# Kernel tuning notes

Measured on AMD Instinct MI355X. Metric: run time of the kernel, lower is better.

## Reference

```python
import jax, jax.numpy as jnp
import numpy as np


def setup_inputs() -> dict:
    key = jax.random.key(0)
    k_x, k_w1, k_b1, k_w2, k_b2 = jax.random.split(key, 5)
    N, D, H = 4_000_000, 10, 16
    x = jax.random.normal(k_x, (N, D), dtype=jnp.float32)
    # torch.nn.Linear default init: U(-1/sqrt(fan_in), 1/sqrt(fan_in))
    lim1 = 1.0 / np.sqrt(D)
    W1 = jax.random.uniform(k_w1, (H, D), minval=-lim1, maxval=lim1, dtype=jnp.float32)
    b1 = jax.random.uniform(k_b1, (H,), minval=-lim1, maxval=lim1, dtype=jnp.float32)
    lim2 = 1.0 / np.sqrt(H)
    W2 = jax.random.uniform(k_w2, (1, H), minval=-lim2, maxval=lim2, dtype=jnp.float32)
    b2 = jax.random.uniform(k_b2, (1,), minval=-lim2, maxval=lim2, dtype=jnp.float32)
    return {"x": x, "W1": W1, "b1": b1, "W2": W2, "b2": b2}


def reference(x, W1, b1, W2, b2):
    # Gram matrix: (10, 10)
    y = x.T @ x
    # symmetric eigendecomposition; w: eigenvectors (10, 10), ascending eigenvalues
    v, w = jnp.linalg.eigh(y)
    h = jax.nn.relu(w @ W1.T + b1)          # (10, 16)
    o = h @ W2.T + b2                        # (10, 1)
    return 0.5 * (jax.nn.sigmoid(o) + 1.0)
```

## Files before the change

### kernel.cpp

```cpp
#include <hip/hip_runtime.h>
#include <math.h>

#pragma clang fp contract(off)

#define NACC 55
#define KC_DEFAULT 384
#define FOLD_LDS 12288

__device__ __forceinline__ void group_load(const float4* __restrict__ xv,
                                           long g, float4* buf) {
#pragma unroll
  for (int t = 0; t < 20; ++t) buf[t] = xv[g * 20 + t];
}

__device__ __forceinline__ void pair_fma_one(const float4 q0, const float4 q1,
                                             const float4 q2, const float4 q3,
                                             const float4 q4, float* acc) {
  float a[10] = {q0.x, q0.y, q0.z, q0.w, q1.x, q1.y, q1.z, q1.w, q2.x, q2.y};
  float b[10] = {q2.z, q2.w, q3.x, q3.y, q3.z, q3.w, q4.x, q4.y, q4.z, q4.w};
  int e = 0;
#pragma unroll
  for (int i = 0; i < 10; ++i)
#pragma unroll
    for (int j = 0; j <= i; ++j) {
      acc[e] = __builtin_fmaf(a[i], a[j], acc[e]);
      acc[e] = __builtin_fmaf(b[i], b[j], acc[e]);
      ++e;
    }
}

__device__ __forceinline__ void group_fma(const float4* buf, float* acc) {
#pragma unroll
  for (int pp = 0; pp < 4; ++pp)
    pair_fma_one(buf[pp * 5 + 0], buf[pp * 5 + 1], buf[pp * 5 + 2],
                 buf[pp * 5 + 3], buf[pp * 5 + 4], acc);
}

__global__ __launch_bounds__(64, 1) void gram32_kernel(
    const float* __restrict__ x, float* __restrict__ partial,
    int nrows, int kc, int nchunks, int prow) {
  int c = blockIdx.x * 64 + threadIdx.x;
  if (c >= nchunks) return;
  long k0 = (long)c * kc;
  long rem = (long)nrows - k0;
  int klen = rem < kc ? (int)rem : kc;

  float acc[NACC];
#pragma unroll
  for (int e = 0; e < NACC; ++e) acc[e] = 0.0f;

  const float4* __restrict__ xv = (const float4*)(x + k0 * 10);
  int npair = klen >> 1;
  int ngrp = npair >> 2;

  float4 bufA[20], bufB[20];

  int g = 0;
  if (ngrp > 0) group_load(xv, 0, bufA);
  while (g < ngrp) {
    if (g + 1 < ngrp) group_load(xv, g + 1, bufB);
    group_fma(bufA, acc);
    ++g;
    if (g >= ngrp) break;
    if (g + 1 < ngrp) group_load(xv, g + 1, bufA);
    group_fma(bufB, acc);
    ++g;
  }
  for (int p = ngrp * 4; p < npair; ++p) {
    float4 v0 = xv[(long)p * 5 + 0];
    float4 v1 = xv[(long)p * 5 + 1];
    float4 v2 = xv[(long)p * 5 + 2];
    float4 v3 = xv[(long)p * 5 + 3];
    float4 v4 = xv[(long)p * 5 + 4];
    pair_fma_one(v0, v1, v2, v3, v4, acc);
  }
  if (klen & 1) {
    const float* row = x + (k0 + klen - 1) * 10;
    float a[10];
#pragma unroll
    for (int i = 0; i < 10; ++i) a[i] = row[i];
    int e = 0;
#pragma unroll
    for (int i = 0; i < 10; ++i)
#pragma unroll
      for (int j = 0; j <= i; ++j) {
        acc[e] = __builtin_fmaf(a[i], a[j], acc[e]);
        ++e;
      }
  }
#pragma unroll
  for (int e = 0; e < NACC; ++e)
    partial[(long)e * prow + c] = acc[e];
}

__global__ __launch_bounds__(256) void fold32_kernel(
    const float* __restrict__ partial, float* __restrict__ G, int nchunks,
    int prow) {
  __shared__ float buf[FOLD_LDS];
  int e = blockIdx.x;
  const float* p = partial + (long)e * prow;

  if (nchunks <= FOLD_LDS) {
    int n4 = nchunks >> 2;
    const float4* p4 = (const float4*)p;
    float4* b4 = (float4*)buf;
    for (int i = threadIdx.x; i < n4; i += 256) b4[i] = p4[i];
    for (int i = (n4 << 2) + threadIdx.x; i < nchunks; i += 256)
      buf[i] = p[i];
    __syncthreads();
    if (threadIdx.x == 0) {
      float s = buf[0];
      int c = 1;
      for (; c + 16 <= nchunks; c += 16) {
        float v[16];
#pragma unroll
        for (int t = 0; t < 16; ++t) v[t] = buf[c + t];
#pragma unroll
        for (int t = 0; t < 16; ++t) s = s + v[t];
      }
      for (; c < nchunks; ++c) s = s + buf[c];
      G[e] = s;
    }
  } else {
    if (threadIdx.x == 0) {
      float s = p[0];
      for (int c = 1; c < nchunks; ++c) s = s + p[c];
      G[e] = s;
    }
  }
}

__device__ __forceinline__ float s_sign(float a, float b) {
  return copysignf(fabsf(a), b);
}
__device__ __forceinline__ float slapy2(float x, float y) {
  float xa = fabsf(x), ya = fabsf(y);
  float w = fmaxf(xa, ya), z = fminf(xa, ya);
  if (z == 0.0f) return w;
  float t = z / w;
  return w * sqrtf(1.0f + t * t);
}
__device__ __forceinline__ void slartg(float f, float g, float* c, float* s,
                                       float* r) {
  if (g == 0.0f) {
    *c = 1.0f; *s = 0.0f; *r = f;
  } else if (f == 0.0f) {
    *c = 0.0f; *s = s_sign(1.0f, g); *r = fabsf(g);
  } else {
    float d = sqrtf(f * f + g * g);
    *c = fabsf(f) / d;
    *r = s_sign(d, f);
    *s = g / (*r);
  }
}
__device__ void slaev2(float a, float b, float c, float* rt1, float* rt2,
                       float* cs1, float* sn1) {
  float sm = a + c, df = a - c;
  float adf = fabsf(df);
  float tb = b + b;
  float ab = fabsf(tb);
  float acmx, acmn;
  if (fabsf(a) > fabsf(c)) { acmx = a; acmn = c; } else { acmx = c; acmn = a; }
  float rt;
  if (adf > ab) { float t = ab / adf; rt = adf * sqrtf(1.0f + t * t); }
  else if (adf < ab) { float t = adf / ab; rt = ab * sqrtf(1.0f + t * t); }
  else rt = ab * sqrtf(2.0f);
  int sgn1;
  if (sm < 0.0f) {
    *rt1 = 0.5f * (sm - rt); sgn1 = -1;
    *rt2 = (acmx / *rt1) * acmn - (b / *rt1) * b;
  } else if (sm > 0.0f) {
    *rt1 = 0.5f * (sm + rt); sgn1 = 1;
    *rt2 = (acmx / *rt1) * acmn - (b / *rt1) * b;
  } else {
    *rt1 = 0.5f * rt; *rt2 = -0.5f * rt; sgn1 = 1;
  }
  int sgn2;
  float cs;
  if (df >= 0.0f) { cs = df + rt; sgn2 = 1; } else { cs = df - rt; sgn2 = -1; }
  float acs = fabsf(cs);
  if (acs > ab) {
    float ct = -tb / cs;
    *sn1 = 1.0f / sqrtf(1.0f + ct * ct);
    *cs1 = ct * (*sn1);
  } else {
    if (ab == 0.0f) { *cs1 = 1.0f; *sn1 = 0.0f; }
    else {
      float tn = -cs / tb;
      *cs1 = 1.0f / sqrtf(1.0f + tn * tn);
      *sn1 = tn * (*cs1);
    }
  }
  if (sgn1 == sgn2) { float tn = *cs1; *cs1 = -(*sn1); *sn1 = tn; }
}

__device__ __forceinline__ float xget(const float* a, int idx) {
  float r = a[0];
#pragma unroll
  for (int k = 1; k < 10; ++k)
    if (idx == k) r = a[k];
  return r;
}
__device__ __forceinline__ void xput(float* a, int idx, float v) {
#pragma unroll
  for (int k = 0; k < 10; ++k)
    if (idx == k) a[k] = v;
}

__global__ __launch_bounds__(64) void solve_kernel(
    const float* __restrict__ Gp, const float* __restrict__ W1,
    const float* __restrict__ b1, const float* __restrict__ W2,
    const float* __restrict__ b2, float* __restrict__ out) {
  const int lane = threadIdx.x;
  const int myrow = lane < 10 ? lane : 9;

  float row[10];
#pragma unroll
  for (int c = 0; c < 10; ++c) {
    int rr = myrow >= c ? myrow : c;
    int cc = myrow >= c ? c : myrow;
    row[c] = Gp[rr * (rr + 1) / 2 + cc];
  }

  float d[10], e[10], tau[9];

#pragma unroll
  for (int i = 0; i < 9; ++i) {
    float v[10];
    {
      float myci = row[i];
#pragma unroll
      for (int k = 0; k < 10; ++k) v[k] = __shfl(myci, k, 64);
    }
    float alpha = v[i + 1];
    float xn2 = 0.0f;
#pragma unroll
    for (int k = i + 2; k < 10; ++k) xn2 = xn2 + v[k] * v[k];
    float xnorm = sqrtf(xn2);
    float taui;
    if (xnorm == 0.0f) {
      taui = 0.0f;
      e[i] = alpha;
    } else {
      float beta = -s_sign(slapy2(alpha, xnorm), alpha);
      taui = (beta - alpha) / beta;
      float sc = 1.0f / (alpha - beta);
#pragma unroll
      for (int k = i + 2; k < 10; ++k) v[k] = v[k] * sc;
      if (lane >= i + 2 && lane < 10) row[i] = row[i] * sc;
      if (lane == i) {
#pragma unroll
        for (int c = i + 2; c < 10; ++c) row[c] = row[c] * sc;
      }
      if (lane == i + 1) row[i] = beta;
      if (lane == i) row[i + 1] = beta;
      e[i] = beta;
    }
    if (taui != 0.0f) {
      v[i + 1] = 1.0f;
      float vme = (lane == i + 1)
                      ? 1.0f
                      : ((lane >= i + 2 && lane < 10) ? row[i] : 0.0f);
      float s = 0.0f;
#pragma unroll
      for (int c2 = i + 1; c2 < 10; ++c2) s = s + row[c2] * v[c2];
      float pvr = taui * s;
      float pva[10];
#pragma unroll
      for (int k = 0; k < 10; ++k) pva[k] = __shfl(pvr, k, 64);
      float dot = 0.0f;
#pragma unroll
      for (int k = i + 1; k < 10; ++k) dot = dot + pva[k] * v[k];
      float alpha2 = -0.5f * taui * dot;
      pvr = pvr + alpha2 * vme;
#pragma unroll
      for (int k = 0; k < 10; ++k) pva[k] = pva[k] + alpha2 * v[k];
      if (lane >= i + 1 && lane < 10) {
#pragma unroll
        for (int c2 = i + 1; c2 < 10; ++c2)
          row[c2] = row[c2] - (vme * pva[c2] + pvr * v[c2]);
      }
    }
    tau[i] = taui;
    d[i] = __shfl(row[i], i, 64);
  }
  d[9] = __shfl(row[9], 9, 64);

  float z[10];
#pragma unroll
  for (int rr2 = 0; rr2 < 10; ++rr2) z[rr2] = (lane == rr2) ? 1.0f : 0.0f;

  const float eps = 5.9604644775390625e-08f;
  const float eps2 = 3.5527136788005009e-15f;
  const float safmin = 1.1754943508222875e-38f;
  const int nmaxit = 300;
  int jtot = 0;
  int l1 = 0;

  while (l1 < 10) {
    if (l1 > 0) xput(e, l1 - 1, 0.0f);
    int m = 9;
    {
      bool fnd = false;
#pragma unroll
      for (int mm = 0; mm < 9; ++mm) {
        if (!fnd && mm >= l1) {
          float tst = fabsf(e[mm]);
          if (tst == 0.0f) {
            m = mm; fnd = true;
          } else if (tst <=
                     (sqrtf(fabsf(d[mm])) * sqrtf(fabsf(d[mm + 1]))) * eps) {
            e[mm] = 0.0f; m = mm; fnd = true;
          }
        }
      }
    }
    int l = l1, lsv = l, lend = m, lendsv = lend;
    l1 = m + 1;
    if (lend == l) continue;
    float anorm = 0.0f;
#pragma unroll
    for (int k = 0; k < 10; ++k)
      if (k >= l && k <= lend) anorm = fmaxf(anorm, fabsf(d[k]));
#pragma unroll
    for (int k = 0; k < 9; ++k)
      if (k >= l && k < lend) anorm = fmaxf(anorm, fabsf(e[k]));
    if (anorm == 0.0f) continue;
    if (fabsf(xget(d, lend)) < fabsf(xget(d, l))) { lend = lsv; l = lendsv; }

    if (lend > l) {
      for (;;) {
        int m2 = lend;
        if (l != lend) {
          bool fnd = false;
#pragma unroll
          for (int mm = 0; mm < 9; ++mm) {
            if (!fnd && mm >= l && mm <= lend - 1) {
              float tst = e[mm] * e[mm];
              if (tst <= (eps2 * fabsf(d[mm])) * fabsf(d[mm + 1]) + safmin) {
                m2 = mm; fnd = true;
              }
            }
          }
        }
        if (m2 < lend) xput(e, m2, 0.0f);
        float p = xget(d, l);
        if (m2 == l) {
          ++l;
          if (l <= lend) continue;
          break;
        }
        if (m2 == l + 1) {
          float rt1, rt2, cc2, ss2;
          slaev2(xget(d, l), xget(e, l), xget(d, l + 1), &rt1, &rt2, &cc2,
                 &ss2);
#pragma unroll
          for (int rr2 = 0; rr2 < 10; ++rr2) {
            float zl = __shfl(z[rr2], l, 64);
            float zl1 = __shfl(z[rr2], l + 1, 64);
            float t = zl1;
            float nj1 = cc2 * t - ss2 * zl;
            float nj = ss2 * t + cc2 * zl;
            if (lane == l) z[rr2] = nj;
            if (lane == l + 1) z[rr2] = nj1;
          }
          xput(d, l, rt1);
          xput(d, l + 1, rt2);
          xput(e, l, 0.0f);
          l += 2;
          if (l <= lend) continue;
          break;
        }
        if (jtot == nmaxit) break;
        ++jtot;
        float g = (xget(d, l + 1) - p) / (2.0f * xget(e, l));
        float r2 = slapy2(g, 1.0f);
        g = xget(d, m2) - p + (xget(e, l) / (g + s_sign(r2, g)));
        float ss = 1.0f, cc = 1.0f;
        p = 0.0f;
        float wcA[10], wsA[10];
#pragma unroll
        for (int i2 = 8; i2 >= 0; --i2) {
          if (i2 >= l && i2 <= m2 - 1) {
            float f = ss * e[i2];
            float bb = cc * e[i2];
            slartg(g, f, &cc, &ss, &r2);
            if (i2 != m2 - 1) e[i2 + 1] = r2;
            g = d[i2 + 1] - p;
            r2 = (d[i2] - g) * ss + 2.0f * cc * bb;
            p = ss * r2;
            d[i2 + 1] = g + p;
            g = cc * r2 - bb;
            wcA[i2] = cc;
            wsA[i2] = -ss;
          }
        }
#pragma unroll
        for (int j = 8; j >= 0; --j) {
          if (j >= l && j <= m2 - 1) {
            float cj = wcA[j], sj = wsA[j];
#pragma unroll
            for (int rr2 = 0; rr2 < 10; ++rr2) {
              float zj = __shfl(z[rr2], j, 64);
              float zj1 = __shfl(z[rr2], j + 1, 64);
              float t = zj1;
              float nj1 = cj * t - sj * zj;
              float nj = sj * t + cj * zj;
              if (lane == j) z[rr2] = nj;
              if (lane == j + 1) z[rr2] = nj1;
            }
          }
        }
        xput(d, l, xget(d, l) - p);
        xput(e, l, g);
      }
    } else {
      for (;;) {
        int m2 = lend;
        if (l != lend) {
          bool fnd = false;
#pragma unroll
          for (int mm = 9; mm >= 1; --mm) {
            if (!fnd && mm <= l && mm >= lend + 1) {
              float tst = e[mm - 1] * e[mm - 1];
              if (tst <= (eps2 * fabsf(d[mm])) * fabsf(d[mm - 1]) + safmin) {
                m2 = mm; fnd = true;
              }
            }
          }
        }
        if (m2 > lend) xput(e, m2 - 1, 0.0f);
        float p = xget(d, l);
        if (m2 == l) {
          --l;
          if (l >= lend) continue;
          break;
        }
        if (m2 == l - 1) {
          float rt1, rt2, cc2, ss2;
          slaev2(xget(d, l - 1), xget(e, l - 1), xget(d, l), &rt1, &rt2, &cc2,
                 &ss2);
#pragma unroll
          for (int rr2 = 0; rr2 < 10; ++rr2) {
            float zl = __shfl(z[rr2], l, 64);
            float zlm = __shfl(z[rr2], l - 1, 64);
            float t = zl;
            float nl = cc2 * t - ss2 * zlm;
            float nlm = ss2 * t + cc2 * zlm;
            if (lane == l) z[rr2] = nl;
            if (lane == l - 1) z[rr2] = nlm;
          }
          xput(d, l - 1, rt1);
          xput(d, l, rt2);
          xput(e, l - 1, 0.0f);
          l -= 2;
          if (l >= lend) continue;
          break;
        }
        if (jtot == nmaxit) break;
        ++jtot;
        float g = (xget(d, l - 1) - p) / (2.0f * xget(e, l - 1));
        float r2 = slapy2(g, 1.0f);
        g = xget(d, m2) - p + (xget(e, l - 1) / (g + s_sign(r2, g)));
        float ss = 1.0f, cc = 1.0f;
        p = 0.0f;
        float wcA[10], wsA[10];
#pragma unroll
        for (int i2 = 0; i2 <= 8; ++i2) {
          if (i2 >= m2 && i2 <= l - 1) {
            float f = ss * e[i2];
            float bb = cc * e[i2];
            slartg(g, f, &cc, &ss, &r2);
            if (i2 != m2) e[(i2 > 0) ? i2 - 1 : 0] = r2;
            g = d[i2] - p;
            r2 = (d[i2 + 1] - g) * ss + 2.0f * cc * bb;
            p = ss * r2;
            d[i2] = g + p;
            g = cc * r2 - bb;
            wcA[i2] = cc;
            wsA[i2] = ss;
          }
        }
#pragma unroll
        for (int j = 0; j <= 8; ++j) {
          if (j >= m2 && j <= l - 1) {
            float cj = wcA[j], sj = wsA[j];
#pragma unroll
            for (int rr2 = 0; rr2 < 10; ++rr2) {
              float zj = __shfl(z[rr2], j, 64);
              float zj1 = __shfl(z[rr2], j + 1, 64);
              float t = zj1;
              float nj1 = cj * t - sj * zj;
              float nj = sj * t + cj * zj;
              if (lane == j) z[rr2] = nj;
              if (lane == j + 1) z[rr2] = nj1;
            }
          }
        }
        xput(d, l, xget(d, l) - p);
        xput(e, l - 1, g);
      }
    }
  }

#pragma unroll
  for (int ii = 1; ii < 10; ++ii) {
    const int i2 = ii - 1;
    int k2 = i2;
    float pmin = d[i2];
#pragma unroll
    for (int j = ii; j < 10; ++j)
      if (d[j] < pmin) { k2 = j; pmin = d[j]; }
    if (k2 != i2) {
      xput(d, k2, d[i2]);
      d[i2] = pmin;
#pragma unroll
      for (int rr2 = 0; rr2 < 10; ++rr2) {
        float zi = __shfl(z[rr2], i2, 64);
        float zk = __shfl(z[rr2], k2, 64);
        if (lane == i2) z[rr2] = zk;
        if (lane == k2) z[rr2] = zi;
      }
    }
  }

#pragma unroll
  for (int i = 8; i >= 0; --i) {
    float taui = tau[i];
    if (taui != 0.0f) {
      float hv[10];
      {
        float myci = row[i];
#pragma unroll
        for (int k = 0; k < 10; ++k) hv[k] = __shfl(myci, k, 64);
      }
      float w = z[i + 1];
#pragma unroll
      for (int k2 = i + 2; k2 < 10; ++k2) w = w + hv[k2] * z[k2];
      w = w * taui;
      z[i + 1] = z[i + 1] - w;
#pragma unroll
      for (int k2 = i + 2; k2 < 10; ++k2) z[k2] = z[k2] - hv[k2] * w;
    }
  }

  float zrow[10];
#pragma unroll
  for (int rr2 = 0; rr2 < 10; ++rr2) {
#pragma unroll
    for (int c = 0; c < 10; ++c) {
      float t = __shfl(z[rr2], c, 64);
      if (lane == rr2) zrow[c] = t;
    }
  }

  if (lane < 10) {
    float o = 0.0f;
#pragma unroll
    for (int j = 0; j < 16; ++j) {
      float acc = 0.0f;
#pragma unroll
      for (int k = 0; k < 10; ++k) acc = acc + zrow[k] * W1[j * 10 + k];
      acc = acc + b1[j];
      float h = fmaxf(acc, 0.0f);
      o = o + h * W2[j];
    }
    o = o + b2[0];
    float sig = 1.0f / (1.0f + expf(-o));
    out[lane] = 0.5f * (sig + 1.0f);
  }
}

extern "C" void kernel_launch(void* const* d_in, const int* in_sizes, int n_in,
                              void* d_out, int out_size, void* d_ws,
                              size_t ws_size, hipStream_t stream) {
  const float* x = (const float*)d_in[0];
  const float* W1 = (const float*)d_in[1];
  const float* b1 = (const float*)d_in[2];
  const float* W2 = (const float*)d_in[3];
  const float* b2 = (const float*)d_in[4];
  float* out = (float*)d_out;

  int nrows = in_sizes[0] / 10;

  int kc = KC_DEFAULT;
  for (;;) {
    long nchunks = ((long)nrows + kc - 1) / kc;
    long prow = (nchunks + 63) & ~63L;
    size_t need = (size_t)NACC * prow * sizeof(float) + 256;
    if (need <= ws_size || kc > nrows) break;
    kc *= 2;
  }
  int nchunks = (int)(((long)nrows + kc - 1) / kc);
  int prow = (int)(((long)nchunks + 63) & ~63L);

  float* partial = (float*)d_ws;
  float* G = partial + (size_t)NACC * prow;

  int grid = (nchunks + 63) / 64;
  gram32_kernel<<<grid, 64, 0, stream>>>(x, partial, nrows, kc, nchunks,
                                         prow);
  fold32_kernel<<<NACC, 256, 0, stream>>>(partial, G, nchunks, prow);
  solve_kernel<<<1, 64, 0, stream>>>(G, W1, b1, W2, b2, out);
}
```

Baseline: 201.0 us.

## Keep eigenvector rows per lane and scalarize tridiagonal state to avoid shuffles

Switches the eigenvector accumulator from a column-per-lane layout to a row-per-lane layout held in named scalar registers, so each Givens rotation becomes local arithmetic instead of twenty cross-lane shuffles. The diagonal, off-diagonal and rotation arrays become scalar registers accessed through select-chain macros to avoid scratch memory for dynamic indexing. A single shuffle-based transpose is added before the Householder back-transformation. The select chains add ALU work per dynamic access and raise register use.

```diff
diff --git a/kernel.cpp b/kernel.cpp
--- a/kernel.cpp
+++ b/kernel.cpp
@@ -194,18 +194,16 @@
   if (sgn1 == sgn2) { float tn = *cs1; *cs1 = -(*sn1); *sn1 = tn; }
 }
 
-__device__ __forceinline__ float xget(const float* a, int idx) {
-  float r = a[0];
-#pragma unroll
-  for (int k = 1; k < 10; ++k)
-    if (idx == k) r = a[k];
-  return r;
-}
-__device__ __forceinline__ void xput(float* a, int idx, float v) {
-#pragma unroll
-  for (int k = 0; k < 10; ++k)
-    if (idx == k) a[k] = v;
-}
+#define GETD(i) ((i)==0?d0:(i)==1?d1:(i)==2?d2:(i)==3?d3:(i)==4?d4:(i)==5?d5:(i)==6?d6:(i)==7?d7:(i)==8?d8:d9)
+#define PUTD(i,v) do{int _i=(i);float _x=(v);d0=(_i==0)?_x:d0;d1=(_i==1)?_x:d1;d2=(_i==2)?_x:d2;d3=(_i==3)?_x:d3;d4=(_i==4)?_x:d4;d5=(_i==5)?_x:d5;d6=(_i==6)?_x:d6;d7=(_i==7)?_x:d7;d8=(_i==8)?_x:d8;d9=(_i==9)?_x:d9;}while(0)
+#define GETE(i) ((i)==0?e0:(i)==1?e1:(i)==2?e2:(i)==3?e3:(i)==4?e4:(i)==5?e5:(i)==6?e6:(i)==7?e7:e8)
+#define PUTE(i,v) do{int _i=(i);float _x=(v);e0=(_i==0)?_x:e0;e1=(_i==1)?_x:e1;e2=(_i==2)?_x:e2;e3=(_i==3)?_x:e3;e4=(_i==4)?_x:e4;e5=(_i==5)?_x:e5;e6=(_i==6)?_x:e6;e7=(_i==7)?_x:e7;e8=(_i==8)?_x:e8;}while(0)
+#define GETWC(i) ((i)==0?wc0:(i)==1?wc1:(i)==2?wc2:(i)==3?wc3:(i)==4?wc4:(i)==5?wc5:(i)==6?wc6:(i)==7?wc7:wc8)
+#define PUTWC(i,v) do{int _i=(i);float _x=(v);wc0=(_i==0)?_x:wc0;wc1=(_i==1)?_x:wc1;wc2=(_i==2)?_x:wc2;wc3=(_i==3)?_x:wc3;wc4=(_i==4)?_x:wc4;wc5=(_i==5)?_x:wc5;wc6=(_i==6)?_x:wc6;wc7=(_i==7)?_x:wc7;wc8=(_i==8)?_x:wc8;}while(0)
+#define GETWS(i) ((i)==0?ws0:(i)==1?ws1:(i)==2?ws2:(i)==3?ws3:(i)==4?ws4:(i)==5?ws5:(i)==6?ws6:(i)==7?ws7:ws8)
+#define PUTWS(i,v) do{int _i=(i);float _x=(v);ws0=(_i==0)?_x:ws0;ws1=(_i==1)?_x:ws1;ws2=(_i==2)?_x:ws2;ws3=(_i==3)?_x:ws3;ws4=(_i==4)?_x:ws4;ws5=(_i==5)?_x:ws5;ws6=(_i==6)?_x:ws6;ws7=(_i==7)?_x:ws7;ws8=(_i==8)?_x:ws8;}while(0)
+#define GETZ(i) ((i)==0?z0:(i)==1?z1:(i)==2?z2:(i)==3?z3:(i)==4?z4:(i)==5?z5:(i)==6?z6:(i)==7?z7:(i)==8?z8:z9)
+#define PUTZ(i,v) do{int _i=(i);float _x=(v);z0=(_i==0)?_x:z0;z1=(_i==1)?_x:z1;z2=(_i==2)?_x:z2;z3=(_i==3)?_x:z3;z4=(_i==4)?_x:z4;z5=(_i==5)?_x:z5;z6=(_i==6)?_x:z6;z7=(_i==7)?_x:z7;z8=(_i==8)?_x:z8;z9=(_i==9)?_x:z9;}while(0)
 
 __global__ __launch_bounds__(64) void solve_kernel(
     const float* __restrict__ Gp, const float* __restrict__ W1,
@@ -222,7 +220,9 @@
     row[c] = Gp[rr * (rr + 1) / 2 + cc];
   }
 
-  float d[10], e[10], tau[9];
+  float d0, d1, d2, d3, d4, d5, d6, d7, d8, d9;
+  float e0, e1, e2, e3, e4, e5, e6, e7, e8;
+  float tau[9];
 
 #pragma unroll
   for (int i = 0; i < 9; ++i) {
@@ -240,7 +240,7 @@
     float taui;
     if (xnorm == 0.0f) {
       taui = 0.0f;
-      e[i] = alpha;
+      PUTE(i, alpha);
     } else {
       float beta = -s_sign(slapy2(alpha, xnorm), alpha);
       taui = (beta - alpha) / beta;
@@ -254,7 +254,7 @@
       }
       if (lane == i + 1) row[i] = beta;
       if (lane == i) row[i + 1] = beta;
-      e[i] = beta;
+      PUTE(i, beta);
     }
     if (taui != 0.0f) {
       v[i + 1] = 1.0f;
@@ -282,13 +282,26 @@
       }
     }
     tau[i] = taui;
-    d[i] = __shfl(row[i], i, 64);
-  }
-  d[9] = __shfl(row[9], 9, 64);
-
-  float z[10];
-#pragma unroll
-  for (int rr2 = 0; rr2 < 10; ++rr2) z[rr2] = (lane == rr2) ? 1.0f : 0.0f;
+    PUTD(i, __shfl(row[i], i, 64));
+  }
+  PUTD(9, __shfl(row[9], 9, 64));
+
+  float z0, z1, z2, z3, z4, z5, z6, z7, z8, z9;
+  z0 = (lane == 0) ? 1.0f : 0.0f;
+  z1 = (lane == 1) ? 1.0f : 0.0f;
+  z2 = (lane == 2) ? 1.0f : 0.0f;
+  z3 = (lane == 3) ? 1.0f : 0.0f;
+  z4 = (lane == 4) ? 1.0f : 0.0f;
+  z5 = (lane == 5) ? 1.0f : 0.0f;
+  z6 = (lane == 6) ? 1.0f : 0.0f;
+  z7 = (lane == 7) ? 1.0f : 0.0f;
+  z8 = (lane == 8) ? 1.0f : 0.0f;
+  z9 = (lane == 9) ? 1.0f : 0.0f;
+
+  float wc0, wc1, wc2, wc3, wc4, wc5, wc6, wc7, wc8;
+  float ws0, ws1, ws2, ws3, ws4, ws5, ws6, ws7, ws8;
+  wc0 = wc1 = wc2 = wc3 = wc4 = wc5 = wc6 = wc7 = wc8 = 0.0f;
+  ws0 = ws1 = ws2 = ws3 = ws4 = ws5 = ws6 = ws7 = ws8 = 0.0f;
 
   const float eps = 5.9604644775390625e-08f;
   const float eps2 = 3.5527136788005009e-15f;
@@ -298,19 +311,20 @@
   int l1 = 0;
 
   while (l1 < 10) {
-    if (l1 > 0) xput(e, l1 - 1, 0.0f);
+    if (l1 > 0) PUTE(l1 - 1, 0.0f);
     int m = 9;
     {
       bool fnd = false;
 #pragma unroll
       for (int mm = 0; mm < 9; ++mm) {
         if (!fnd && mm >= l1) {
-          float tst = fabsf(e[mm]);
+          float tst = fabsf(GETE(mm));
           if (tst == 0.0f) {
             m = mm; fnd = true;
           } else if (tst <=
-                     (sqrtf(fabsf(d[mm])) * sqrtf(fabsf(d[mm + 1]))) * eps) {
-            e[mm] = 0.0f; m = mm; fnd = true;
+                     (sqrtf(fabsf(GETD(mm))) * sqrtf(fabsf(GETD(mm + 1)))) *
+                         eps) {
+            PUTE(mm, 0.0f); m = mm; fnd = true;
           }
         }
       }
@@ -321,12 +335,12 @@
     float anorm = 0.0f;
 #pragma unroll
     for (int k = 0; k < 10; ++k)
-      if (k >= l && k <= lend) anorm = fmaxf(anorm, fabsf(d[k]));
+      if (k >= l && k <= lend) anorm = fmaxf(anorm, fabsf(GETD(k)));
 #pragma unroll
     for (int k = 0; k < 9; ++k)
-      if (k >= l && k < lend) anorm = fmaxf(anorm, fabsf(e[k]));
+      if (k >= l && k < lend) anorm = fmaxf(anorm, fabsf(GETE(k)));
     if (anorm == 0.0f) continue;
-    if (fabsf(xget(d, lend)) < fabsf(xget(d, l))) { lend = lsv; l = lendsv; }
+    if (fabsf(GETD(lend)) < fabsf(GETD(l))) { lend = lsv; l = lendsv; }
 
     if (lend > l) {
       for (;;) {
@@ -336,15 +350,16 @@
 #pragma unroll
           for (int mm = 0; mm < 9; ++mm) {
             if (!fnd && mm >= l && mm <= lend - 1) {
-              float tst = e[mm] * e[mm];
-              if (tst <= (eps2 * fabsf(d[mm])) * fabsf(d[mm + 1]) + safmin) {
+              float tst = GETE(mm) * GETE(mm);
+              if (tst <=
+                  (eps2 * fabsf(GETD(mm))) * fabsf(GETD(mm + 1)) + safmin) {
                 m2 = mm; fnd = true;
               }
             }
           }
         }
-        if (m2 < lend) xput(e, m2, 0.0f);
-        float p = xget(d, l);
+        if (m2 < lend) PUTE(m2, 0.0f);
+        float p = GETD(l);
         if (m2 == l) {
           ++l;
           if (l <= lend) continue;
@@ -352,67 +367,57 @@
         }
         if (m2 == l + 1) {
           float rt1, rt2, cc2, ss2;
-          slaev2(xget(d, l), xget(e, l), xget(d, l + 1), &rt1, &rt2, &cc2,
-                 &ss2);
-#pragma unroll
-          for (int rr2 = 0; rr2 < 10; ++rr2) {
-            float zl = __shfl(z[rr2], l, 64);
-            float zl1 = __shfl(z[rr2], l + 1, 64);
+          slaev2(GETD(l), GETE(l), GETD(l + 1), &rt1, &rt2, &cc2, &ss2);
+          {
+            float zl = GETZ(l), zl1 = GETZ(l + 1);
             float t = zl1;
-            float nj1 = cc2 * t - ss2 * zl;
-            float nj = ss2 * t + cc2 * zl;
-            if (lane == l) z[rr2] = nj;
-            if (lane == l + 1) z[rr2] = nj1;
-          }
-          xput(d, l, rt1);
-          xput(d, l + 1, rt2);
-          xput(e, l, 0.0f);
+            float nl1 = cc2 * t - ss2 * zl;
+            float nl = ss2 * t + cc2 * zl;
+            PUTZ(l + 1, nl1);
+            PUTZ(l, nl);
+          }
+          PUTD(l, rt1);
+          PUTD(l + 1, rt2);
+          PUTE(l, 0.0f);
           l += 2;
           if (l <= lend) continue;
           break;
         }
         if (jtot == nmaxit) break;
         ++jtot;
-        float g = (xget(d, l + 1) - p) / (2.0f * xget(e, l));
+        float g = (GETD(l + 1) - p) / (2.0f * GETE(l));
         float r2 = slapy2(g, 1.0f);
-        g = xget(d, m2) - p + (xget(e, l) / (g + s_sign(r2, g)));
+        g = GETD(m2) - p + (GETE(l) / (g + s_sign(r2, g)));
         float ss = 1.0f, cc = 1.0f;
         p = 0.0f;
-        float wcA[10], wsA[10];
 #pragma unroll
         for (int i2 = 8; i2 >= 0; --i2) {
           if (i2 >= l && i2 <= m2 - 1) {
-            float f = ss * e[i2];
-            float bb = cc * e[i2];
+            float f = ss * GETE(i2);
+            float bb = cc * GETE(i2);
             slartg(g, f, &cc, &ss, &r2);
-            if (i2 != m2 - 1) e[i2 + 1] = r2;
-            g = d[i2 + 1] - p;
-            r2 = (d[i2] - g) * ss + 2.0f * cc * bb;
+            if (i2 != m2 - 1) PUTE(i2 + 1, r2);
+            g = GETD(i2 + 1) - p;
+            r2 = (GETD(i2) - g) * ss + 2.0f * cc * bb;
             p = ss * r2;
-            d[i2 + 1] = g + p;
+            PUTD(i2 + 1, g + p);
             g = cc * r2 - bb;
-            wcA[i2] = cc;
-            wsA[i2] = -ss;
+            PUTWC(i2, cc);
+            PUTWS(i2, -ss);
           }
         }
 #pragma unroll
         for (int j = 8; j >= 0; --j) {
           if (j >= l && j <= m2 - 1) {
-            float cj = wcA[j], sj = wsA[j];
-#pragma unroll
-            for (int rr2 = 0; rr2 < 10; ++rr2) {
-              float zj = __shfl(z[rr2], j, 64);
-              float zj1 = __shfl(z[rr2], j + 1, 64);
-              float t = zj1;
-              float nj1 = cj * t - sj * zj;
-              float nj = sj * t + cj * zj;
-              if (lane == j) z[rr2] = nj;
-              if (lane == j + 1) z[rr2] = nj1;
-            }
-          }
-        }
-        xput(d, l, xget(d, l) - p);
-        xput(e, l, g);
+            float cj = GETWC(j), sj = GETWS(j);
+            float t = GETZ(j + 1);
+            float zj = GETZ(j);
+            PUTZ(j + 1, cj * t - sj * zj);
+            PUTZ(j, sj * t + cj * zj);
+          }
+        }
+        PUTD(l, GETD(l) - p);
+        PUTE(l, g);
       }
     } else {
       for (;;) {
@@ -422,15 +427,16 @@
 #pragma unroll
           for (int mm = 9; mm >= 1; --mm) {
             if (!fnd && mm <= l && mm >= lend + 1) {
-              float tst = e[mm - 1] * e[mm - 1];
-              if (tst <= (eps2 * fabsf(d[mm])) * fabsf(d[mm - 1]) + safmin) {
+              float tst = GETE(mm - 1) * GETE(mm - 1);
+              if (tst <=
+                  (eps2 * fabsf(GETD(mm))) * fabsf(GETD(mm - 1)) + safmin) {
                 m2 = mm; fnd = true;
               }
             }
           }
         }
-        if (m2 > lend) xput(e, m2 - 1, 0.0f);
-        float p = xget(d, l);
+        if (m2 > lend) PUTE(m2 - 1, 0.0f);
+        float p = GETD(l);
         if (m2 == l) {
           --l;
           if (l >= lend) continue;
@@ -438,67 +444,57 @@
         }
         if (m2 == l - 1) {
           float rt1, rt2, cc2, ss2;
-          slaev2(xget(d, l - 1), xget(e, l - 1), xget(d, l), &rt1, &rt2, &cc2,
-                 &ss2);
-#pragma unroll
-          for (int rr2 = 0; rr2 < 10; ++rr2) {
-            float zl = __shfl(z[rr2], l, 64);
-            float zlm = __shfl(z[rr2], l - 1, 64);
+          slaev2(GETD(l - 1), GETE(l - 1), GETD(l), &rt1, &rt2, &cc2, &ss2);
+          {
+            float zl = GETZ(l), zlm = GETZ(l - 1);
             float t = zl;
             float nl = cc2 * t - ss2 * zlm;
             float nlm = ss2 * t + cc2 * zlm;
-            if (lane == l) z[rr2] = nl;
-            if (lane == l - 1) z[rr2] = nlm;
-          }
-          xput(d, l - 1, rt1);
-          xput(d, l, rt2);
-          xput(e, l - 1, 0.0f);
+            PUTZ(l, nl);
+            PUTZ(l - 1, nlm);
+          }
+          PUTD(l - 1, rt1);
+          PUTD(l, rt2);
+          PUTE(l - 1, 0.0f);
           l -= 2;
           if (l >= lend) continue;
           break;
         }
         if (jtot == nmaxit) break;
         ++jtot;
-        float g = (xget(d, l - 1) - p) / (2.0f * xget(e, l - 1));
+        float g = (GETD(l - 1) - p) / (2.0f * GETE(l - 1));
         float r2 = slapy2(g, 1.0f);
-        g = xget(d, m2) - p + (xget(e, l - 1) / (g + s_sign(r2, g)));
+        g = GETD(m2) - p + (GETE(l - 1) / (g + s_sign(r2, g)));
         float ss = 1.0f, cc = 1.0f;
         p = 0.0f;
-        float wcA[10], wsA[10];
 #pragma unroll
         for (int i2 = 0; i2 <= 8; ++i2) {
           if (i2 >= m2 && i2 <= l - 1) {
-            float f = ss * e[i2];
-            float bb = cc * e[i2];
+            float f = ss * GETE(i2);
+            float bb = cc * GETE(i2);
             slartg(g, f, &cc, &ss, &r2);
-            if (i2 != m2) e[(i2 > 0) ? i2 - 1 : 0] = r2;
-            g = d[i2] - p;
-            r2 = (d[i2 + 1] - g) * ss + 2.0f * cc * bb;
+            if (i2 != m2) PUTE(i2 - 1, r2);
+            g = GETD(i2) - p;
+            r2 = (GETD(i2 + 1) - g) * ss + 2.0f * cc * bb;
             p = ss * r2;
-            d[i2] = g + p;
+            PUTD(i2, g + p);
             g = cc * r2 - bb;
-            wcA[i2] = cc;
-            wsA[i2] = ss;
+            PUTWC(i2, cc);
+            PUTWS(i2, ss);
           }
         }
 #pragma unroll
         for (int j = 0; j <= 8; ++j) {
           if (j >= m2 && j <= l - 1) {
-            float cj = wcA[j], sj = wsA[j];
-#pragma unroll
-            for (int rr2 = 0; rr2 < 10; ++rr2) {
-              float zj = __shfl(z[rr2], j, 64);
-              float zj1 = __shfl(z[rr2], j + 1, 64);
-              float t = zj1;
-              float nj1 = cj * t - sj * zj;
-              float nj = sj * t + cj * zj;
-              if (lane == j) z[rr2] = nj;
-              if (lane == j + 1) z[rr2] = nj1;
-            }
-          }
-        }
-        xput(d, l, xget(d, l) - p);
-        xput(e, l - 1, g);
+            float cj = GETWC(j), sj = GETWS(j);
+            float t = GETZ(j + 1);
+            float zj = GETZ(j);
+            PUTZ(j + 1, cj * t - sj * zj);
+            PUTZ(j, sj * t + cj * zj);
+          }
+        }
+        PUTD(l, GETD(l) - p);
+        PUTE(l - 1, g);
       }
     }
   }
@@ -507,19 +503,33 @@
   for (int ii = 1; ii < 10; ++ii) {
     const int i2 = ii - 1;
     int k2 = i2;
-    float pmin = d[i2];
-#pragma unroll
-    for (int j = ii; j < 10; ++j)
-      if (d[j] < pmin) { k2 = j; pmin = d[j]; }
+    float pmin = GETD(i2);
+#pragma unroll
+    for (int j = ii; j < 10; ++j) {
+      float dj = GETD(j);
+      if (dj < pmin) { k2 = j; pmin = dj; }
+    }
     if (k2 != i2) {
-      xput(d, k2, d[i2]);
-      d[i2] = pmin;
-#pragma unroll
-      for (int rr2 = 0; rr2 < 10; ++rr2) {
-        float zi = __shfl(z[rr2], i2, 64);
-        float zk = __shfl(z[rr2], k2, 64);
-        if (lane == i2) z[rr2] = zk;
-        if (lane == k2) z[rr2] = zi;
+      PUTD(k2, GETD(i2));
+      PUTD(i2, pmin);
+      float ti = GETZ(i2);
+      float tk = GETZ(k2);
+      PUTZ(i2, tk);
+      PUTZ(k2, ti);
+    }
+  }
+
+  float zc[10];
+#pragma unroll
+  for (int r = 0; r < 10; ++r) zc[r] = 0.0f;
+  {
+    float zreg[10] = {z0, z1, z2, z3, z4, z5, z6, z7, z8, z9};
+#pragma unroll
+    for (int r = 0; r < 10; ++r) {
+#pragma unroll
+      for (int c = 0; c < 10; ++c) {
+        float t = __shfl(zreg[c], r, 64);
+        zc[r] = (lane == c) ? t : zc[r];
       }
     }
   }
@@ -534,23 +544,25 @@
 #pragma unroll
         for (int k = 0; k < 10; ++k) hv[k] = __shfl(myci, k, 64);
       }
-      float w = z[i + 1];
-#pragma unroll
-      for (int k2 = i + 2; k2 < 10; ++k2) w = w + hv[k2] * z[k2];
+      float w = zc[i + 1];
+#pragma unroll
+      for (int k2 = i + 2; k2 < 10; ++k2) w = w + hv[k2] * zc[k2];
       w = w * taui;
-      z[i + 1] = z[i + 1] - w;
-#pragma unroll
-      for (int k2 = i + 2; k2 < 10; ++k2) z[k2] = z[k2] - hv[k2] * w;
+      zc[i + 1] = zc[i + 1] - w;
+#pragma unroll
+      for (int k2 = i + 2; k2 < 10; ++k2) zc[k2] = zc[k2] - hv[k2] * w;
     }
   }
 
   float zrow[10];
 #pragma unroll
-  for (int rr2 = 0; rr2 < 10; ++rr2) {
+  for (int c = 0; c < 10; ++c) zrow[c] = 0.0f;
+#pragma unroll
+  for (int r = 0; r < 10; ++r) {
 #pragma unroll
     for (int c = 0; c < 10; ++c) {
-      float t = __shfl(z[rr2], c, 64);
-      if (lane == rr2) zrow[c] = t;
+      float t = __shfl(zc[r], c, 64);
+      zrow[c] = (lane == r) ? t : zrow[c];
     }
   }
 
```

Result: faster. 180.9 us (-10.0%).
